# Performance work log

Measured on AMD Instinct MI355X. Metric: run time of the kernel, lower is better.

## Reference

```python
import jax, jax.numpy as jnp
import numpy as np

VOCAB = 5000
HIDDEN = 512
BATCH = 64
SEQ = 256


def setup_inputs() -> dict:
    key = jax.random.key(0)
    ks = jax.random.split(key, 8)
    s = 0.02
    return {
        "X": jax.random.randint(ks[0], (BATCH, SEQ), 0, VOCAB),
        "state": jnp.zeros((1, BATCH, HIDDEN), jnp.float32),
        # PyTorch GRU params: weight_ih (3H, V), weight_hh (3H, H), biases (3H,)
        "W_ih": jax.random.normal(ks[1], (3 * HIDDEN, VOCAB), jnp.float32) * s,
        "W_hh": jax.random.normal(ks[2], (3 * HIDDEN, HIDDEN), jnp.float32) * s,
        "b_ih": jax.random.normal(ks[3], (3 * HIDDEN,), jnp.float32) * s,
        "b_hh": jax.random.normal(ks[4], (3 * HIDDEN,), jnp.float32) * s,
        # dense: Linear(hidden, vocab)
        "W_out": jax.random.normal(ks[5], (VOCAB, HIDDEN), jnp.float32) * s,
        "b_out": jax.random.normal(ks[6], (VOCAB,), jnp.float32) * s,
    }


def reference(X, state, W_ih, W_hh, b_ih, b_hh, W_out, b_out):
    V = W_ih.shape[1]
    H = W_hh.shape[1]
    # d2l.to_onehot + torch.stack -> (seq, batch, vocab), seq-first for GRU
    onehot = jax.nn.one_hot(X.T, V, dtype=W_ih.dtype)  # (S, B, V)
    # input-side GEMM for all timesteps at once (cuDNN does the same batching)
    x_proj = jnp.einsum('sbv,gv->sbg', onehot, W_ih) + b_ih  # (S, B, 3H)

    h0 = state[0]  # (B, H)

    def step(h, xp):
        gi_r, gi_z, gi_n = jnp.split(xp, 3, axis=-1)
        gh = h @ W_hh.T + b_hh
        gh_r, gh_z, gh_n = jnp.split(gh, 3, axis=-1)
        r = jax.nn.sigmoid(gi_r + gh_r)
        z = jax.nn.sigmoid(gi_z + gh_z)
        n = jnp.tanh(gi_n + r * gh_n)
        h_new = (1.0 - z) * n + z * h
        return h_new, h_new

    hT, Y = jax.lax.scan(step, h0, x_proj)  # Y: (S, B, H)
    out = Y.reshape(-1, H) @ W_out.T + b_out  # (S*B, V)
    return out, hT[None]  # state shape (1, B, H)
```

## Files before the change

### kernel.cpp

```cpp
#include <hip/hip_runtime.h>

typedef __attribute__((ext_vector_type(8))) short bf16x8;
typedef __attribute__((ext_vector_type(4))) float f32x4;
typedef __attribute__((ext_vector_type(4))) int i32x4;
typedef __attribute__((ext_vector_type(2))) unsigned int u32x2;
typedef unsigned short ushort_t;
typedef unsigned int uint_t;

#define VOCAB 5000
#define HID   512
#define B_    64
#define SEQ_  256
#define H3    1536
#define NPAD  5120
#define NREC  32
#define NGEM  224
#define NTILE (SEQ_ * 40)

__device__ __forceinline__ ushort_t f2bf(float f){
  uint_t u = __float_as_uint(f);
  u = u + 0x7fffu + ((u >> 16) & 1u);
  return (ushort_t)(u >> 16);
}
__device__ __forceinline__ float bf2f(ushort_t s){
  return __uint_as_float(((uint_t)s) << 16);
}

__device__ __forceinline__ uint_t agent_load_u32(const uint_t* p){
  uint_t v;
  asm volatile("global_load_dword %0, %1, off sc1\n\t"
               "s_waitcnt vmcnt(0)" : "=v"(v) : "v"(p) : "memory");
  return v;
}
__device__ __forceinline__ void agent_store_u32(uint_t* p, uint_t v){
  asm volatile("global_store_dword %0, %1, off sc1" :: "v"(p), "v"(v) : "memory");
}
__device__ __forceinline__ void agent_store_u64(ushort_t* p, u32x2 v){
  asm volatile("global_store_dwordx2 %0, %1, off sc1" :: "v"(p), "v"(v) : "memory");
}

__global__ void k_transpose(const float* __restrict__ W, float* __restrict__ WT){
  __shared__ float tile[32][33];
  const int bv = blockIdx.x * 32;
  const int bg = blockIdx.y * 32;
  const int tx = threadIdx.x, ty = threadIdx.y;
  #pragma unroll
  for(int r = 0; r < 32; r += 8){
    int g = bg + ty + r, v = bv + tx;
    tile[ty + r][tx] = (v < VOCAB) ? W[(size_t)g * VOCAB + v] : 0.f;
  }
  __syncthreads();
  #pragma unroll
  for(int r = 0; r < 32; r += 8){
    int v = bv + ty + r, g = bg + tx;
    if(v < VOCAB) WT[(size_t)v * H3 + g] = tile[tx][ty + r];
  }
}

__global__ void k_cvt_wout(const float* __restrict__ W, ushort_t* __restrict__ WP){
  int idx = (blockIdx.x * 256 + threadIdx.x) * 4;
  if(idx >= NPAD * HID) return;
  float x0 = 0.f, x1 = 0.f, x2 = 0.f, x3 = 0.f;
  if(idx < VOCAB * HID){
    const float4 v = *(const float4*)(W + idx);
    x0 = v.x; x1 = v.y; x2 = v.z; x3 = v.w;
  }
  ushort4 o; o.x = f2bf(x0); o.y = f2bf(x1); o.z = f2bf(x2); o.w = f2bf(x3);
  *(ushort4*)(WP + idx) = o;
}

__global__ void k_gather(const int* __restrict__ X, const float* __restrict__ WT,
                         const float* __restrict__ bih, ushort_t* __restrict__ xp){
  const int sb = blockIdx.x;
  const int s = sb >> 6, b = sb & 63;
  const int x = X[b * SEQ_ + s];
  const float4* src = (const float4*)(WT + (size_t)x * H3);
  const float4* bi  = (const float4*)bih;
  for(int i = threadIdx.x; i < H3 / 4; i += 256){
    float4 v = src[i], c = bi[i];
    ushort4 o;
    o.x = f2bf(v.x + c.x); o.y = f2bf(v.y + c.y);
    o.z = f2bf(v.z + c.z); o.w = f2bf(v.w + c.w);
    ((ushort4*)(xp + (size_t)sb * H3))[i] = o;
  }
}

__global__ void __launch_bounds__(256, 1) k_mega(
    const float* __restrict__ Whh, const float* __restrict__ bhh,
    const float* __restrict__ state, const ushort_t* __restrict__ xp,
    const ushort_t* __restrict__ WP, const float* __restrict__ bout,
    ushort_t* __restrict__ hbuf, ushort_t* __restrict__ Y,
    float* __restrict__ out, float* __restrict__ hT, uint_t* flags)
{
  __shared__ __align__(16) char smem[102912];
  const int bid = blockIdx.x, tid = threadIdx.x;
  const int lane = tid & 63, wv = tid >> 6;
  const int l15 = lane & 15, lhi = lane >> 4;

  if(bid < NREC){
    ushort_t (*Wl)[520] = (ushort_t(*)[520])smem;
    float* bl = (float*)(smem + 96 * 520 * 2);
    ushort_t (*tsc)[16][20] = (ushort_t(*)[16][20])(smem + 100224);
    const int g = bid;
    const int dom = g >> 4, sub = g & 15;
    const int jb = sub * 32;

    for(int idx = tid; idx < 96 * 512; idx += 256){
      int r = idx >> 9, c = idx & 511;
      int jgr = r / 48, rem = r % 48;
      int gate = rem >> 4, jl = jgr * 16 + (rem & 15);
      Wl[r][c] = f2bf(Whh[((size_t)(gate * HID + jb + jl)) * HID + c]);
    }
    if(tid < 96){
      int jgr = tid / 48, rem = tid % 48;
      int gate = rem >> 4, jl = jgr * 16 + (rem & 15);
      bl[tid] = bhh[gate * HID + jb + jl];
    }

    const int jg = wv >> 1;
    const int jt0 = jb + jg * 16;
    const int j  = jt0 + l15;
    const int rbase = jg * 48;
    const int bband = dom * 32 + (wv & 1) * 16;

    float hprev[4]; int brow[4];
    #pragma unroll
    for(int i = 0; i < 4; i++){
      brow[i] = bband + lhi * 4 + i;
      hprev[i] = state[brow[i] * HID + j];
    }

    #pragma unroll
    for(int i = 0; i < 4; i++) tsc[wv][lhi * 4 + i][l15] = f2bf(hprev[i]);
    asm volatile("s_waitcnt lgkmcnt(0)" ::: "memory");
    {
      u32x2 rv = *(const u32x2*)&tsc[wv][l15][lhi * 4];
      agent_store_u64(hbuf + (size_t)(bband + l15) * HID + jt0 + lhi * 4, rv);
    }
    asm volatile("s_waitcnt vmcnt(0)" ::: "memory");
    __syncthreads();
    if(tid == 0) agent_store_u32(flags + g * 32, 1u);

    const int fidx = dom * 16 + ((lane + sub) & 15);

    for(int t = 0; t < SEQ_; ++t){
      const ushort_t* hin  = hbuf + (t & 1) * (B_ * HID);
      ushort_t*       hout = hbuf + ((t + 1) & 1) * (B_ * HID);

      float gir[4], giz[4], gin_[4];
      const ushort_t* xr = xp + (size_t)t * B_ * H3;
      #pragma unroll
      for(int i = 0; i < 4; i++){
        const ushort_t* p = xr + (size_t)brow[i] * H3 + j;
        gir[i] = bf2f(p[0]); giz[i] = bf2f(p[HID]); gin_[i] = bf2f(p[2 * HID]);
      }

      if(lane < 16){
        const uint_t need = (uint_t)(t + 1);
        int gd = 0;
        while(agent_load_u32(flags + fidx * 32) < need){
          __builtin_amdgcn_s_sleep(1);
          if(++gd > 200000) break;
        }
      }

      i32x4 tmp[16];
      const char* abase = (const char*)(hin + (size_t)(bband + l15) * HID + 8 * lhi);
      #define LDH(i, off) asm volatile("global_load_dwordx4 %0, %1, off offset:" #off " sc1" \
                                       : "=v"(tmp[i]) : "v"(abase) : "memory");
      LDH(0,0)   LDH(1,64)   LDH(2,128)  LDH(3,192)
      LDH(4,256) LDH(5,320)  LDH(6,384)  LDH(7,448)
      LDH(8,512) LDH(9,576)  LDH(10,640) LDH(11,704)
      LDH(12,768) LDH(13,832) LDH(14,896) LDH(15,960)
      #undef LDH
      asm volatile("s_waitcnt vmcnt(0)" ::: "memory");
      __builtin_amdgcn_sched_barrier(0);

      f32x4 acc0 = {0.f,0.f,0.f,0.f}, acc1 = {0.f,0.f,0.f,0.f}, acc2 = {0.f,0.f,0.f,0.f};
      #pragma unroll
      for(int kk = 0; kk < 16; kk++){
        bf16x8 a = __builtin_bit_cast(bf16x8, tmp[kk]);
        const int kc = kk * 32 + 8 * lhi;
        bf16x8 b0 = *(const bf16x8*)&Wl[rbase + l15][kc];
        bf16x8 b1 = *(const bf16x8*)&Wl[rbase + 16 + l15][kc];
        bf16x8 b2 = *(const bf16x8*)&Wl[rbase + 32 + l15][kc];
        acc0 = __builtin_amdgcn_mfma_f32_16x16x32_bf16(a, b0, acc0, 0, 0, 0);
        acc1 = __builtin_amdgcn_mfma_f32_16x16x32_bf16(a, b1, acc1, 0, 0, 0);
        acc2 = __builtin_amdgcn_mfma_f32_16x16x32_bf16(a, b2, acc2, 0, 0, 0);
      }

      const float cr = bl[rbase + l15], cz = bl[rbase + 16 + l15], cn = bl[rbase + 32 + l15];
      float hn4[4];
      #pragma unroll
      for(int i = 0; i < 4; i++){
        float r = 1.f / (1.f + expf(-(gir[i] + acc0[i] + cr)));
        float z = 1.f / (1.f + expf(-(giz[i] + acc1[i] + cz)));
        float n = tanhf(gin_[i] + r * (acc2[i] + cn));
        hn4[i] = (1.f - z) * n + z * hprev[i];
        hprev[i] = hn4[i];
      }

      #pragma unroll
      for(int i = 0; i < 4; i++) tsc[wv][lhi * 4 + i][l15] = f2bf(hn4[i]);
      asm volatile("s_waitcnt lgkmcnt(0)" ::: "memory");
      {
        u32x2 rv = *(const u32x2*)&tsc[wv][l15][lhi * 4];
        const size_t roff = (size_t)(bband + l15) * HID + jt0 + lhi * 4;
        agent_store_u64(hout + roff, rv);
        agent_store_u64(Y + (size_t)t * B_ * HID + roff, rv);
      }
      asm volatile("s_waitcnt vmcnt(0)" ::: "memory");
      __syncthreads();
      if(tid == 0) agent_store_u32(flags + g * 32, (uint_t)(t + 2));

      if(t == SEQ_ - 1){
        #pragma unroll
        for(int i = 0; i < 4; i++) hT[brow[i] * HID + j] = hn4[i];
      }
    }
  } else {
    ushort_t (*At)[520] = (ushort_t(*)[520])smem;
    const int gb = bid - NREC;

    for(int tile = gb; tile < NTILE; tile += NGEM){
      const int t = tile / 40, n0 = (tile % 40) * 128;

      if(wv == 0){
        const uint_t need = (uint_t)(t + 2);
        int gd = 0;
        while(true){
          uint_t v = 0xffffffffu;
          if(lane < 32) v = agent_load_u32(flags + lane * 32);
          if(__all(v >= need)) break;
          __builtin_amdgcn_s_sleep(64);
          if(++gd > 2000000) break;
        }
      }
      __syncthreads();

      {
        const int row = tid >> 2, q = tid & 3;
        const char* src = (const char*)(Y + (size_t)t * B_ * HID) + row * 1024 + q * 256;
        i32x4 tv[16];
        #define LDA(i, off) asm volatile("global_load_dwordx4 %0, %1, off offset:" #off " sc1" \
                                         : "=v"(tv[i]) : "v"(src) : "memory");
        LDA(0,0)   LDA(1,16)  LDA(2,32)  LDA(3,48)
        LDA(4,64)  LDA(5,80)  LDA(6,96)  LDA(7,112)
        LDA(8,128) LDA(9,144) LDA(10,160) LDA(11,176)
        LDA(12,192) LDA(13,208) LDA(14,224) LDA(15,240)
        #undef LDA
        asm volatile("s_waitcnt vmcnt(0)" ::: "memory");
        __builtin_amdgcn_sched_barrier(0);
        #pragma unroll
        for(int i = 0; i < 16; i++) *(i32x4*)&At[row][q * 128 + i * 8] = tv[i];
      }
      __syncthreads();

      f32x4 acc[4][2];
      #pragma unroll
      for(int a = 0; a < 4; a++){ acc[a][0] = (f32x4){0,0,0,0}; acc[a][1] = (f32x4){0,0,0,0}; }

      const ushort_t* B0 = WP + (size_t)(n0 + wv * 32 + l15) * HID;
      const ushort_t* B1 = WP + (size_t)(n0 + wv * 32 + 16 + l15) * HID;
      #pragma unroll
      for(int kt = 0; kt < 16; kt++){
        const int kc = kt * 32 + 8 * lhi;
        bf16x8 b0 = *(const bf16x8*)(B0 + kc);
        bf16x8 b1 = *(const bf16x8*)(B1 + kc);
        bf16x8 a0 = *(const bf16x8*)&At[0 * 16 + l15][kc];
        bf16x8 a1 = *(const bf16x8*)&At[1 * 16 + l15][kc];
        bf16x8 a2 = *(const bf16x8*)&At[2 * 16 + l15][kc];
        bf16x8 a3 = *(const bf16x8*)&At[3 * 16 + l15][kc];
        acc[0][0] = __builtin_amdgcn_mfma_f32_16x16x32_bf16(a0, b0, acc[0][0], 0, 0, 0);
        acc[0][1] = __builtin_amdgcn_mfma_f32_16x16x32_bf16(a0, b1, acc[0][1], 0, 0, 0);
        acc[1][0] = __builtin_amdgcn_mfma_f32_16x16x32_bf16(a1, b0, acc[1][0], 0, 0, 0);
        acc[1][1] = __builtin_amdgcn_mfma_f32_16x16x32_bf16(a1, b1, acc[1][1], 0, 0, 0);
        acc[2][0] = __builtin_amdgcn_mfma_f32_16x16x32_bf16(a2, b0, acc[2][0], 0, 0, 0);
        acc[2][1] = __builtin_amdgcn_mfma_f32_16x16x32_bf16(a2, b1, acc[2][1], 0, 0, 0);
        acc[3][0] = __builtin_amdgcn_mfma_f32_16x16x32_bf16(a3, b0, acc[3][0], 0, 0, 0);
        acc[3][1] = __builtin_amdgcn_mfma_f32_16x16x32_bf16(a3, b1, acc[3][1], 0, 0, 0);
      }

      #pragma unroll
      for(int mi = 0; mi < 4; mi++){
        #pragma unroll
        for(int ni = 0; ni < 2; ni++){
          const int v = n0 + wv * 32 + ni * 16 + l15;
          if(v < VOCAB){
            const float bb = bout[v];
            #pragma unroll
            for(int i = 0; i < 4; i++){
              const int sb = t * 64 + mi * 16 + lhi * 4 + i;
              out[(size_t)sb * VOCAB + v] = acc[mi][ni][i] + bb;
            }
          }
        }
      }
      __syncthreads();
    }
  }
}

extern "C" void kernel_launch(void* const* d_in, const int* in_sizes, int n_in,
                              void* d_out, int out_size, void* d_ws, size_t ws_size,
                              hipStream_t stream)
{
  const int*   X     = (const int*)  d_in[0];
  const float* state = (const float*)d_in[1];
  const float* Wih   = (const float*)d_in[2];
  const float* Whh   = (const float*)d_in[3];
  const float* bih   = (const float*)d_in[4];
  const float* bhh   = (const float*)d_in[5];
  const float* Wout  = (const float*)d_in[6];
  const float* bout  = (const float*)d_in[7];
  float* out = (float*)d_out;
  float* hT  = out + (size_t)SEQ_ * B_ * VOCAB;

  char* ws = (char*)d_ws;
  const size_t off_WihT  = 4096;
  const size_t off_WoutP = off_WihT  + (size_t)VOCAB * H3  * sizeof(float);
  const size_t off_Y     = off_WoutP + (size_t)NPAD  * HID * sizeof(ushort_t);
  const size_t off_h     = off_Y     + (size_t)SEQ_ * B_ * HID * sizeof(ushort_t);
  const size_t off_xp    = off_h     + (size_t)2 * B_ * HID * sizeof(ushort_t);

  uint_t*   flags = (uint_t*)  ws;
  float*    WihT  = (float*)   (ws + off_WihT);
  ushort_t* WoutP = (ushort_t*)(ws + off_WoutP);
  ushort_t* Ybuf  = (ushort_t*)(ws + off_Y);
  ushort_t* hbuf  = (ushort_t*)(ws + off_h);
  ushort_t* xp    = (ushort_t*)(ws + off_xp);

  (void)hipMemsetAsync(d_ws, 0, 4096, stream);
  hipLaunchKernelGGL(k_transpose, dim3(157, 48), dim3(32, 8), 0, stream, Wih, WihT);
  hipLaunchKernelGGL(k_cvt_wout, dim3((NPAD * HID / 4 + 255) / 256), dim3(256), 0, stream, Wout, WoutP);
  hipLaunchKernelGGL(k_gather, dim3(SEQ_ * B_), dim3(256), 0, stream, X, WihT, bih, xp);
  hipLaunchKernelGGL(k_mega, dim3(NREC + NGEM), dim3(256), 0, stream,
                     Whh, bhh, state, xp, WoutP, bout, hbuf, Ybuf, out, hT, flags);
}
```

Measured before the change: 1.290 ms.

## Keep recurrent W_hh slice in registers and repartition recurrent blocks

Recurrent blocks now cover 16 batch rows by 64 hidden units instead of 32 by 32, and each warp preloads its three gate weight fragments as bf16 into registers rather than staging them in shared memory. This removes per-timestep LDS reads of the weight operand and the shared bias array. The flag polling is narrowed to the 8 producer blocks each domain depends on. It raises register pressure sharply, with a risk of spills.

Measured after the change: 1.211 ms (median of 2 runs). 6.1% less time.

```diff
diff --git a/kernel.cpp b/kernel.cpp
--- a/kernel.cpp
+++ b/kernel.cpp
@@ -98,30 +98,33 @@
   const int l15 = lane & 15, lhi = lane >> 4;
 
   if(bid < NREC){
-    ushort_t (*Wl)[520] = (ushort_t(*)[520])smem;
-    float* bl = (float*)(smem + 96 * 520 * 2);
     ushort_t (*tsc)[16][20] = (ushort_t(*)[16][20])(smem + 100224);
     const int g = bid;
-    const int dom = g >> 4, sub = g & 15;
-    const int jb = sub * 32;
-
-    for(int idx = tid; idx < 96 * 512; idx += 256){
-      int r = idx >> 9, c = idx & 511;
-      int jgr = r / 48, rem = r % 48;
-      int gate = rem >> 4, jl = jgr * 16 + (rem & 15);
-      Wl[r][c] = f2bf(Whh[((size_t)(gate * HID + jb + jl)) * HID + c]);
-    }
-    if(tid < 96){
-      int jgr = tid / 48, rem = tid % 48;
-      int gate = rem >> 4, jl = jgr * 16 + (rem & 15);
-      bl[tid] = bhh[gate * HID + jb + jl];
-    }
-
-    const int jg = wv >> 1;
-    const int jt0 = jb + jg * 16;
+    const int dom = g >> 3, sub = g & 7;
+    const int jbwg = sub * 64;
+    const int jg = wv;
+    const int jt0 = jbwg + jg * 16;
     const int j  = jt0 + l15;
-    const int rbase = jg * 48;
-    const int bband = dom * 32 + (wv & 1) * 16;
+    const int bband = dom * 16;
+
+    const float cr = bhh[j], cz = bhh[HID + j], cn = bhh[2 * HID + j];
+
+    bf16x8 wb[48];
+    #pragma unroll
+    for(int gate = 0; gate < 3; gate++){
+      #pragma unroll
+      for(int kk = 0; kk < 16; kk++){
+        const float* wsrc = Whh + (size_t)(gate * HID + j) * HID + kk * 32 + 8 * lhi;
+        float4 w0 = *(const float4*)(wsrc);
+        float4 w1 = *(const float4*)(wsrc + 4);
+        bf16x8 bf;
+        bf[0] = (short)f2bf(w0.x); bf[1] = (short)f2bf(w0.y);
+        bf[2] = (short)f2bf(w0.z); bf[3] = (short)f2bf(w0.w);
+        bf[4] = (short)f2bf(w1.x); bf[5] = (short)f2bf(w1.y);
+        bf[6] = (short)f2bf(w1.z); bf[7] = (short)f2bf(w1.w);
+        wb[gate * 16 + kk] = bf;
+      }
+    }
 
     float hprev[4]; int brow[4];
     #pragma unroll
@@ -141,7 +144,8 @@
     __syncthreads();
     if(tid == 0) agent_store_u32(flags + g * 32, 1u);
 
-    const int fidx = dom * 16 + ((lane + sub) & 15);
+    const int fidx = dom * 8 + ((lane + sub) & 7);
+    const size_t roff = (size_t)(bband + l15) * HID + jt0 + lhi * 4;
 
     for(int t = 0; t < SEQ_; ++t){
       const ushort_t* hin  = hbuf + (t & 1) * (B_ * HID);
@@ -155,7 +159,7 @@
         gir[i] = bf2f(p[0]); giz[i] = bf2f(p[HID]); gin_[i] = bf2f(p[2 * HID]);
       }
 
-      if(lane < 16){
+      if(lane < 8){
         const uint_t need = (uint_t)(t + 1);
         int gd = 0;
         while(agent_load_u32(flags + fidx * 32) < need){
@@ -180,16 +184,11 @@
       #pragma unroll
       for(int kk = 0; kk < 16; kk++){
         bf16x8 a = __builtin_bit_cast(bf16x8, tmp[kk]);
-        const int kc = kk * 32 + 8 * lhi;
-        bf16x8 b0 = *(const bf16x8*)&Wl[rbase + l15][kc];
-        bf16x8 b1 = *(const bf16x8*)&Wl[rbase + 16 + l15][kc];
-        bf16x8 b2 = *(const bf16x8*)&Wl[rbase + 32 + l15][kc];
-        acc0 = __builtin_amdgcn_mfma_f32_16x16x32_bf16(a, b0, acc0, 0, 0, 0);
-        acc1 = __builtin_amdgcn_mfma_f32_16x16x32_bf16(a, b1, acc1, 0, 0, 0);
-        acc2 = __builtin_amdgcn_mfma_f32_16x16x32_bf16(a, b2, acc2, 0, 0, 0);
-      }
-
-      const float cr = bl[rbase + l15], cz = bl[rbase + 16 + l15], cn = bl[rbase + 32 + l15];
+        acc0 = __builtin_amdgcn_mfma_f32_16x16x32_bf16(a, wb[kk],      acc0, 0, 0, 0);
+        acc1 = __builtin_amdgcn_mfma_f32_16x16x32_bf16(a, wb[16 + kk], acc1, 0, 0, 0);
+        acc2 = __builtin_amdgcn_mfma_f32_16x16x32_bf16(a, wb[32 + kk], acc2, 0, 0, 0);
+      }
+
       float hn4[4];
       #pragma unroll
       for(int i = 0; i < 4; i++){
@@ -205,7 +204,6 @@
       asm volatile("s_waitcnt lgkmcnt(0)" ::: "memory");
       {
         u32x2 rv = *(const u32x2*)&tsc[wv][l15][lhi * 4];
-        const size_t roff = (size_t)(bband + l15) * HID + jt0 + lhi * 4;
         agent_store_u64(hout + roff, rv);
         agent_store_u64(Y + (size_t)t * B_ * HID + roff, rv);
       }
```
